# Kernel optimization log

Hardware: AMD Instinct MI355X
Metric: run time of the kernel (lower is better)

Reference implementation:

```python
import jax, jax.numpy as jnp
import numpy as np

# ---- Cl(4,1) Cayley table (signature [1,1,1,1,-1]), basis blades indexed by 5-bit mask ----
_METRIC = np.array([1, 1, 1, 1, -1], dtype=np.float32)

def _build_gp_map():
    T = np.zeros((32, 32, 32), dtype=np.float32)
    for a in range(32):
        for b in range(32):
            # canonical reordering sign (count generator swaps)
            s, aa = 0, a >> 1
            while aa:
                s += bin(aa & b).count('1')
                aa >>= 1
            sign = -1.0 if (s & 1) else 1.0
            # metric contribution of annihilated common generators
            common = a & b
            for i in range(5):
                if (common >> i) & 1:
                    sign *= _METRIC[i]
            T[a, b, a ^ b] = sign  # e_a * e_b = sign * e_{a XOR b}
    return T

GP_MAP = _build_gp_map()  # [32, 32, 32], one signed nonzero per (a,b) pair

IN_FEATURES = 256
OUT_FEATURES = 256
BATCH, SEQ = 4, 512


def setup_inputs() -> dict:
    key = jax.random.key(0)
    kx, kw = jax.random.split(key)
    x = jax.random.normal(kx, (BATCH, SEQ, IN_FEATURES, 32), dtype=jnp.float32)
    # Versor init: std = sqrt(2 / (fan_in * 32))
    std = (2.0 / (IN_FEATURES * 32)) ** 0.5
    weight = jax.random.normal(kw, (OUT_FEATURES, IN_FEATURES, 32), dtype=jnp.float32) * std
    return {"x": x, "weight": weight}


def normalize_cl41(out, eps=1e-6):
    # Normalize each output multivector by its Euclidean norm over the 32 basis coeffs.
    norm = jnp.sqrt(jnp.sum(out * out, axis=-1, keepdims=True) + eps)
    return out / norm


def reference(x, weight):
    gp = jnp.asarray(GP_MAP, dtype=x.dtype)  # [j, l, k]
    # W_op[o,i,l,k] = sum_j weight[o,i,j] * gp[j,l,k]
    W_op = jnp.einsum('oij,jlk->oilk', weight, gp)
    # out[b,s,o,k] = sum_{i,l} x[b,s,i,l] * W_op[o,i,l,k]
    out = jnp.einsum('bsil,oilk->bsok', x, W_op)
    return normalize_cl41(out)
```

## Files before the change

kernel.cpp:

```cpp
#include <hip/hip_runtime.h>
#include <stdint.h>

#define AS1 __attribute__((address_space(1)))
#define AS3 __attribute__((address_space(3)))

typedef __attribute__((ext_vector_type(8))) short bf16x8;
typedef __attribute__((ext_vector_type(4))) float f32x4;


struct Mono { int col[4]; int ph[4]; };

constexpr Mono mono_mul(Mono A, Mono B) {
    Mono R{};
    for (int r = 0; r < 4; ++r) {
        int k = A.col[r];
        R.col[r] = B.col[k];
        R.ph[r] = (A.ph[r] + B.ph[k]) & 3;
    }
    return R;
}

constexpr Mono gen(int g) {
    Mono E{};
    for (int r = 0; r < 4; ++r) {
        int r1 = (r >> 1) & 1, r0 = r & 1;
        if (g == 0)      { E.col[r] = r ^ 2; E.ph[r] = 0; }
        else if (g == 1) { E.col[r] = r ^ 2; E.ph[r] = r1 ? 1 : 3; }
        else if (g == 2) { E.col[r] = r ^ 1; E.ph[r] = r1 ? 2 : 0; }
        else if (g == 3) { E.col[r] = r ^ 1; E.ph[r] = ((r1 ? 2 : 0) + (r0 ? 1 : 3)) & 3; }
        else             { E.col[r] = r;     E.ph[r] = (1 + (r1 ? 2 : 0) + (r0 ? 2 : 0)) & 3; }
    }
    return E;
}

struct Blades { Mono m[32]; };
constexpr Blades make_blades() {
    Blades B{};
    for (int A = 0; A < 32; ++A) {
        Mono M{};
        for (int r = 0; r < 4; ++r) { M.col[r] = r; M.ph[r] = 0; }
        for (int g = 0; g < 5; ++g)
            if ((A >> g) & 1) M = mono_mul(M, gen(g));
        B.m[A] = M;
    }
    return B;
}
constexpr Blades BL = make_blades();

struct FwdTab { int bl[4][4][2][4]; float sg[4][4][2][4]; };
constexpr FwdTab make_fwd() {
    FwdTab T{};
    int cnt[4][4][2] = {};
    for (int A = 0; A < 32; ++A)
        for (int r = 0; r < 4; ++r) {
            int c = BL.m[A].col[r], p = BL.m[A].ph[r];
            int rc = p & 1;
            int& n = cnt[r][c][rc];
            T.bl[r][c][rc][n] = A;
            T.sg[r][c][rc][n] = (p & 2) ? -1.f : 1.f;
            ++n;
        }
    return T;
}
constexpr FwdTab FT = make_fwd();

__device__ inline unsigned short f2bf(float f) {
    uint32_t u = __float_as_uint(f);
    u += 0x7FFFu + ((u >> 16) & 1u);
    return (unsigned short)(u >> 16);
}

__global__ __launch_bounds__(256) void xform_kernel(const float* __restrict__ x,
                                                    const float* __restrict__ w,
                                                    unsigned short* __restrict__ Xb,
                                                    unsigned short* __restrict__ Wr) {
    if (blockIdx.x < 2048) {
        int t = blockIdx.x * 256 + threadIdx.x;
        int i = t & 255, n = t >> 8;
        float v[32];
        const float4* xp = (const float4*)(x + (size_t)t * 32);
#pragma unroll
        for (int q = 0; q < 8; ++q) {
            float4 f = xp[q];
            v[q * 4 + 0] = f.x; v[q * 4 + 1] = f.y; v[q * 4 + 2] = f.z; v[q * 4 + 3] = f.w;
        }
#pragma unroll
        for (int b = 0; b < 4; ++b) {
            union { unsigned short s[8]; uint4 u; } r;
#pragma unroll
            for (int c = 0; c < 4; ++c)
#pragma unroll
                for (int rc = 0; rc < 2; ++rc) {
                    float s = 0.f;
#pragma unroll
                    for (int j = 0; j < 4; ++j)
                        s += FT.sg[c][b][rc][j] * v[FT.bl[c][b][rc][j]];
                    r.s[c * 2 + rc] = f2bf(s);
                }
            *((uint4*)(Xb + (size_t)(n * 4 + b) * 2048 + i * 8)) = r.u;
        }
    } else {
        int t = (blockIdx.x - 2048) * 256 + threadIdx.x;
        int i = t & 255, o = t >> 8;
        float v[32];
        const float4* wp = (const float4*)(w + (size_t)t * 32);
#pragma unroll
        for (int q = 0; q < 8; ++q) {
            float4 f = wp[q];
            v[q * 4 + 0] = f.x; v[q * 4 + 1] = f.y; v[q * 4 + 2] = f.z; v[q * 4 + 3] = f.w;
        }
        float Re[4][4], Im[4][4];
#pragma unroll
        for (int a = 0; a < 4; ++a)
#pragma unroll
            for (int c = 0; c < 4; ++c) {
                float sr = 0.f, si = 0.f;
#pragma unroll
                for (int j = 0; j < 4; ++j) {
                    sr += FT.sg[a][c][0][j] * v[FT.bl[a][c][0][j]];
                    si += FT.sg[a][c][1][j] * v[FT.bl[a][c][1][j]];
                }
                Re[a][c] = sr; Im[a][c] = si;
            }
#pragma unroll
        for (int ra = 0; ra < 2; ++ra)
#pragma unroll
            for (int a = 0; a < 4; ++a) {
                int m = o * 8 + ra * 4 + a;
                union { unsigned short s[8]; uint4 u; } r;
#pragma unroll
                for (int c = 0; c < 4; ++c) {
                    float v0 = ra == 0 ? Re[a][c] : Im[a][c];
                    float v1 = ra == 0 ? -Im[a][c] : Re[a][c];
                    r.s[c * 2 + 0] = f2bf(v0);
                    r.s[c * 2 + 1] = f2bf(v1);
                }
                *((uint4*)(Wr + (size_t)m * 2048 + i * 8)) = r.u;
            }
    }
}

__global__ __launch_bounds__(512, 2) void gemm_kernel(const unsigned short* __restrict__ A,
                                                      const unsigned short* __restrict__ B,
                                                      float* __restrict__ out) {
    const int K = 2048;
    const int NT = 64;
    __shared__ alignas(16) unsigned short SM[4 * 16384];

    const int tid = threadIdx.x;
    const int wid = tid >> 6, lane = tid & 63;
    const int lm = lane & 15, quad = lane >> 4;
    const int wm = wid >> 2, wn = wid & 3;
    const int row0 = blockIdx.y * 256;
    const int col0 = blockIdx.x * 256;

    size_t gA[2], gB[2];
    int ldsA[2], ldsB[2];
#pragma unroll
    for (int p = 0; p < 2; ++p) {
        int g = p * 512 + tid;
        int r = g >> 2, c = g & 3;
        int sc = c ^ ((r >> 1) & 3);
        gA[p] = (size_t)(row0 + r) * K + sc * 8;
        gB[p] = (size_t)(col0 + r) * K + sc * 8;
        ldsA[p] = (p * 512 + wid * 64) * 8;
        ldsB[p] = 8192 + (p * 512 + wid * 64) * 8;
    }

    const int swz = (lm >> 1) & 3;
    const int aoff = (wm * 128 + lm) * 32 + (quad ^ swz) * 8;
    const int boff = 8192 + (wn * 64 + lm) * 32 + (quad ^ swz) * 8;

    f32x4 acc[8][4];
#pragma unroll
    for (int i = 0; i < 8; ++i)
#pragma unroll
        for (int j = 0; j < 4; ++j) acc[i][j] = (f32x4){0.f, 0.f, 0.f, 0.f};

    auto ISSUE = [&](int t) {
        const int bb = (t & 3) * 16384;
        const int k0 = t * 32;
#pragma unroll
        for (int p = 0; p < 2; ++p) {
            __builtin_amdgcn_global_load_lds((const AS1 void*)(A + gA[p] + k0),
                                             (AS3 void*)(&SM[bb + ldsA[p]]), 16, 0, 0);
            __builtin_amdgcn_global_load_lds((const AS1 void*)(B + gB[p] + k0),
                                             (AS3 void*)(&SM[bb + ldsB[p]]), 16, 0, 0);
        }
    };
    auto COMPUTE = [&](int t) {
        const int bb = (t & 3) * 16384;
        bf16x8 av[8], bv[4];
#pragma unroll
        for (int fn = 0; fn < 4; ++fn) bv[fn] = *(const bf16x8*)&SM[bb + boff + fn * 512];
#pragma unroll
        for (int fm = 0; fm < 8; ++fm) av[fm] = *(const bf16x8*)&SM[bb + aoff + fm * 512];
        __builtin_amdgcn_s_setprio(1);
#pragma unroll
        for (int fm = 0; fm < 8; ++fm)
#pragma unroll
            for (int fn = 0; fn < 4; ++fn)
                acc[fm][fn] = __builtin_amdgcn_mfma_f32_16x16x32_bf16(av[fm], bv[fn],
                                                                      acc[fm][fn], 0, 0, 0);
        __builtin_amdgcn_s_setprio(0);
    };

    ISSUE(0); ISSUE(1); ISSUE(2);
    for (int t = 0; t < NT - 3; ++t) {
        asm volatile("s_waitcnt vmcnt(8)" ::: "memory");
        __builtin_amdgcn_s_barrier();
        ISSUE(t + 3);
        COMPUTE(t);
    }
    asm volatile("s_waitcnt vmcnt(8)" ::: "memory");
    __builtin_amdgcn_s_barrier();
    COMPUTE(NT - 3);
    asm volatile("s_waitcnt vmcnt(4)" ::: "memory");
    __builtin_amdgcn_s_barrier();
    COMPUTE(NT - 2);
    asm volatile("s_waitcnt vmcnt(0)" ::: "memory");
    __builtin_amdgcn_s_barrier();
    COMPUTE(NT - 1);
    __syncthreads();

    float* scrw = (float*)SM + wid * 2048;
    const int nl = lane >> 2, ol = lane & 3;
#pragma unroll
    for (int s = 0; s < 4; ++s) {
#pragma unroll
        for (int h = 0; h < 2; ++h)
#pragma unroll
            for (int fn = 0; fn < 4; ++fn)
#pragma unroll
                for (int r = 0; r < 4; ++r) {
                    int rw = h * 16 + quad * 4 + r;
                    int cc = (fn * 16 + lm) ^ (quad << 3);
                    scrw[rw * 64 + cc] = acc[s * 2 + h][fn][r];
                }
        asm volatile("s_waitcnt lgkmcnt(0)" ::: "memory");
        float V[32];
#pragma unroll
        for (int u = 0; u < 8; ++u) {
            int row = ol * 8 + u;
            int cb = (nl * 4) ^ (((row >> 2) & 3) << 3);
            float4 f = *(const float4*)&scrw[row * 64 + cb];
            int vi = (u >> 2) * 16 + (u & 3) * 4;
            V[vi + 0] = f.x; V[vi + 1] = f.y; V[vi + 2] = f.z; V[vi + 3] = f.w;
        }
        float xa[32];
        float ss = 0.f;
#pragma unroll
        for (int Ab = 0; Ab < 32; ++Ab) {
            float sv = 0.f;
#pragma unroll
            for (int a = 0; a < 4; ++a) {
                const int c = BL.m[Ab].col[a];
                const int p = BL.m[Ab].ph[a];
                float vv = V[(p & 1) * 16 + a * 4 + c];
                sv += (p & 2) ? -vv : vv;
            }
            sv *= 0.25f;
            xa[Ab] = sv;
            ss += sv * sv;
        }
        float inv = rsqrtf(ss + 1e-6f);
        int o = (row0 >> 3) + wm * 16 + s * 4 + ol;
        int n = (col0 >> 2) + wn * 16 + nl;
        float4* op = (float4*)(out + ((size_t)n * 256 + o) * 32);
#pragma unroll
        for (int q = 0; q < 8; ++q) {
            float4 f;
            f.x = xa[q * 4 + 0] * inv; f.y = xa[q * 4 + 1] * inv;
            f.z = xa[q * 4 + 2] * inv; f.w = xa[q * 4 + 3] * inv;
            op[q] = f;
        }
        asm volatile("s_waitcnt lgkmcnt(0)" ::: "memory");
    }
}

extern "C" void kernel_launch(void* const* d_in, const int* in_sizes, int n_in,
                              void* d_out, int out_size, void* d_ws, size_t ws_size,
                              hipStream_t stream) {
    const float* x = (const float*)d_in[0];
    const float* w = (const float*)d_in[1];
    float* out = (float*)d_out;

    unsigned short* Wr = (unsigned short*)d_ws;
    unsigned short* Xb = (unsigned short*)((char*)d_ws + 8388608);

    hipLaunchKernelGGL(xform_kernel, dim3(2304),  dim3(256), 0, stream, x, w, Xb, Wr);
    hipLaunchKernelGGL(gemm_kernel,  dim3(32, 8), dim3(512), 0, stream, Wr, Xb, out);
}
```

Before: 194.0 us.

## Restructure GEMM main loop into double-buffered split-slot pipeline; coalesce xform loads via LDS

The GEMM main loop moves from a 4-deep ring of K=32 tiles to two 64-wide K buffers, each split into four slots (A/B halves). Each slot's global-to-LDS load is issued in between half-tile MFMA groups, with extra barriers so loads interleave with compute at a finer grain. The xform kernel now stages x through swizzled shared memory so global reads are fully coalesced instead of per-thread 128-byte strided reads. This adds more barriers per iteration and a shallower prefetch distance in the GEMM, which could expose memory latency.

```diff
diff --git a/kernel.cpp b/kernel.cpp
--- a/kernel.cpp
+++ b/kernel.cpp
@@ -6,7 +6,6 @@
 
 typedef __attribute__((ext_vector_type(8))) short bf16x8;
 typedef __attribute__((ext_vector_type(4))) float f32x4;
-
 
 struct Mono { int col[4]; int ph[4]; };
 
@@ -74,16 +73,29 @@
                                                     const float* __restrict__ w,
                                                     unsigned short* __restrict__ Xb,
                                                     unsigned short* __restrict__ Wr) {
+    __shared__ alignas(16) float XS[8192];
     if (blockIdx.x < 2048) {
-        int t = blockIdx.x * 256 + threadIdx.x;
+        int tid = threadIdx.x;
+        const float4* xp = (const float4*)(x + (size_t)blockIdx.x * 8192);
+        float4 ld[8];
+#pragma unroll
+        for (int r = 0; r < 8; ++r) ld[r] = xp[r * 256 + tid];
+#pragma unroll
+        for (int r = 0; r < 8; ++r) {
+            int U = r * 256 + tid;
+            int L = (U & ~7) | ((U & 7) ^ ((U >> 3) & 7));
+            *(float4*)&XS[L * 4] = ld[r];
+        }
+        __syncthreads();
+        float v[32];
+#pragma unroll
+        for (int q = 0; q < 8; ++q) {
+            int L = tid * 8 + (q ^ (tid & 7));
+            float4 f = *(const float4*)&XS[L * 4];
+            v[q * 4 + 0] = f.x; v[q * 4 + 1] = f.y; v[q * 4 + 2] = f.z; v[q * 4 + 3] = f.w;
+        }
+        int t = blockIdx.x * 256 + tid;
         int i = t & 255, n = t >> 8;
-        float v[32];
-        const float4* xp = (const float4*)(x + (size_t)t * 32);
-#pragma unroll
-        for (int q = 0; q < 8; ++q) {
-            float4 f = xp[q];
-            v[q * 4 + 0] = f.x; v[q * 4 + 1] = f.y; v[q * 4 + 2] = f.z; v[q * 4 + 3] = f.w;
-        }
 #pragma unroll
         for (int b = 0; b < 4; ++b) {
             union { unsigned short s[8]; uint4 u; } r;
@@ -144,8 +156,7 @@
                                                       const unsigned short* __restrict__ B,
                                                       float* __restrict__ out) {
     const int K = 2048;
-    const int NT = 64;
-    __shared__ alignas(16) unsigned short SM[4 * 16384];
+    __shared__ alignas(16) unsigned short SM[65536];
 
     const int tid = threadIdx.x;
     const int wid = tid >> 6, lane = tid & 63;
@@ -155,21 +166,17 @@
     const int col0 = blockIdx.x * 256;
 
     size_t gA[2], gB[2];
-    int ldsA[2], ldsB[2];
 #pragma unroll
     for (int p = 0; p < 2; ++p) {
-        int g = p * 512 + tid;
-        int r = g >> 2, c = g & 3;
-        int sc = c ^ ((r >> 1) & 3);
-        gA[p] = (size_t)(row0 + r) * K + sc * 8;
-        gB[p] = (size_t)(col0 + r) * K + sc * 8;
-        ldsA[p] = (p * 512 + wid * 64) * 8;
-        ldsB[p] = 8192 + (p * 512 + wid * 64) * 8;
+        int u = p * 512 + tid;
+        int r = u >> 2, j = (u & 3) ^ ((r >> 1) & 3);
+        gA[p] = (size_t)(row0 + r) * K + j * 8;
+        gB[p] = (size_t)(col0 + r) * K + j * 8;
     }
 
     const int swz = (lm >> 1) & 3;
     const int aoff = (wm * 128 + lm) * 32 + (quad ^ swz) * 8;
-    const int boff = 8192 + (wn * 64 + lm) * 32 + (quad ^ swz) * 8;
+    const int boff = (wn * 64 + lm) * 32 + (quad ^ swz) * 8;
 
     f32x4 acc[8][4];
 #pragma unroll
@@ -177,50 +184,128 @@
 #pragma unroll
         for (int j = 0; j < 4; ++j) acc[i][j] = (f32x4){0.f, 0.f, 0.f, 0.f};
 
-    auto ISSUE = [&](int t) {
-        const int bb = (t & 3) * 16384;
-        const int k0 = t * 32;
-#pragma unroll
-        for (int p = 0; p < 2; ++p) {
-            __builtin_amdgcn_global_load_lds((const AS1 void*)(A + gA[p] + k0),
-                                             (AS3 void*)(&SM[bb + ldsA[p]]), 16, 0, 0);
-            __builtin_amdgcn_global_load_lds((const AS1 void*)(B + gB[p] + k0),
-                                             (AS3 void*)(&SM[bb + ldsB[p]]), 16, 0, 0);
-        }
+    auto STAGE = [&](int tt, int slot) {
+        const int ks = slot >> 1;
+        const size_t ko = (size_t)tt * 64 + ks * 32;
+        const int dst = (tt & 1) * 32768 + slot * 8192;
+        const unsigned short* base = (slot & 1) ? B : A;
+        const size_t g0 = (slot & 1) ? gB[0] : gA[0];
+        const size_t g1 = (slot & 1) ? gB[1] : gA[1];
+        __builtin_amdgcn_global_load_lds((const AS1 void*)(base + g0 + ko),
+                                         (AS3 void*)&SM[dst + wid * 512], 16, 0, 0);
+        __builtin_amdgcn_global_load_lds((const AS1 void*)(base + g1 + ko),
+                                         (AS3 void*)&SM[dst + 4096 + wid * 512], 16, 0, 0);
     };
-    auto COMPUTE = [&](int t) {
-        const int bb = (t & 3) * 16384;
-        bf16x8 av[8], bv[4];
-#pragma unroll
-        for (int fn = 0; fn < 4; ++fn) bv[fn] = *(const bf16x8*)&SM[bb + boff + fn * 512];
-#pragma unroll
-        for (int fm = 0; fm < 8; ++fm) av[fm] = *(const bf16x8*)&SM[bb + aoff + fm * 512];
-        __builtin_amdgcn_s_setprio(1);
-#pragma unroll
-        for (int fm = 0; fm < 8; ++fm)
-#pragma unroll
-            for (int fn = 0; fn < 4; ++fn)
-                acc[fm][fn] = __builtin_amdgcn_mfma_f32_16x16x32_bf16(av[fm], bv[fn],
-                                                                      acc[fm][fn], 0, 0, 0);
-        __builtin_amdgcn_s_setprio(0);
-    };
-
-    ISSUE(0); ISSUE(1); ISSUE(2);
-    for (int t = 0; t < NT - 3; ++t) {
-        asm volatile("s_waitcnt vmcnt(8)" ::: "memory");
-        __builtin_amdgcn_s_barrier();
-        ISSUE(t + 3);
-        COMPUTE(t);
-    }
-    asm volatile("s_waitcnt vmcnt(8)" ::: "memory");
-    __builtin_amdgcn_s_barrier();
-    COMPUTE(NT - 3);
-    asm volatile("s_waitcnt vmcnt(4)" ::: "memory");
-    __builtin_amdgcn_s_barrier();
-    COMPUTE(NT - 2);
-    asm volatile("s_waitcnt vmcnt(0)" ::: "memory");
-    __builtin_amdgcn_s_barrier();
-    COMPUTE(NT - 1);
+
+    STAGE(0, 0); STAGE(0, 1); STAGE(0, 2); STAGE(0, 3);
+
+    bf16x8 a0[4], a1[4], bv[4];
+    for (int t = 0; t < 31; ++t) {
+        const int bb = (t & 1) * 32768;
+        asm volatile("s_waitcnt vmcnt(4)" ::: "memory");
+        __builtin_amdgcn_s_barrier();
+#pragma unroll
+        for (int f = 0; f < 4; ++f) a0[f] = *(const bf16x8*)&SM[bb + aoff + f * 512];
+#pragma unroll
+        for (int f = 0; f < 4; ++f) bv[f] = *(const bf16x8*)&SM[bb + 8192 + boff + f * 512];
+        STAGE(t + 1, 0);
+        __builtin_amdgcn_s_barrier();
+        __builtin_amdgcn_s_setprio(1);
+#pragma unroll
+        for (int f = 0; f < 4; ++f)
+#pragma unroll
+            for (int n = 0; n < 4; ++n)
+                acc[f][n] = __builtin_amdgcn_mfma_f32_16x16x32_bf16(a0[f], bv[n], acc[f][n], 0, 0, 0);
+        __builtin_amdgcn_s_setprio(0);
+#pragma unroll
+        for (int f = 0; f < 4; ++f) a1[f] = *(const bf16x8*)&SM[bb + aoff + (f + 4) * 512];
+        STAGE(t + 1, 1);
+        __builtin_amdgcn_s_barrier();
+        __builtin_amdgcn_s_setprio(1);
+#pragma unroll
+        for (int f = 0; f < 4; ++f)
+#pragma unroll
+            for (int n = 0; n < 4; ++n)
+                acc[f + 4][n] = __builtin_amdgcn_mfma_f32_16x16x32_bf16(a1[f], bv[n], acc[f + 4][n], 0, 0, 0);
+        __builtin_amdgcn_s_setprio(0);
+        asm volatile("s_waitcnt vmcnt(4)" ::: "memory");
+        __builtin_amdgcn_s_barrier();
+#pragma unroll
+        for (int f = 0; f < 4; ++f) a0[f] = *(const bf16x8*)&SM[bb + 16384 + aoff + f * 512];
+#pragma unroll
+        for (int f = 0; f < 4; ++f) bv[f] = *(const bf16x8*)&SM[bb + 24576 + boff + f * 512];
+        STAGE(t + 1, 2);
+        __builtin_amdgcn_s_barrier();
+        __builtin_amdgcn_s_setprio(1);
+#pragma unroll
+        for (int f = 0; f < 4; ++f)
+#pragma unroll
+            for (int n = 0; n < 4; ++n)
+                acc[f][n] = __builtin_amdgcn_mfma_f32_16x16x32_bf16(a0[f], bv[n], acc[f][n], 0, 0, 0);
+        __builtin_amdgcn_s_setprio(0);
+#pragma unroll
+        for (int f = 0; f < 4; ++f) a1[f] = *(const bf16x8*)&SM[bb + 16384 + aoff + (f + 4) * 512];
+        STAGE(t + 1, 3);
+        __builtin_amdgcn_s_barrier();
+        __builtin_amdgcn_s_setprio(1);
+#pragma unroll
+        for (int f = 0; f < 4; ++f)
+#pragma unroll
+            for (int n = 0; n < 4; ++n)
+                acc[f + 4][n] = __builtin_amdgcn_mfma_f32_16x16x32_bf16(a1[f], bv[n], acc[f + 4][n], 0, 0, 0);
+        __builtin_amdgcn_s_setprio(0);
+    }
+    {
+        const int bb = 32768;
+        asm volatile("s_waitcnt vmcnt(4)" ::: "memory");
+        __builtin_amdgcn_s_barrier();
+#pragma unroll
+        for (int f = 0; f < 4; ++f) a0[f] = *(const bf16x8*)&SM[bb + aoff + f * 512];
+#pragma unroll
+        for (int f = 0; f < 4; ++f) bv[f] = *(const bf16x8*)&SM[bb + 8192 + boff + f * 512];
+        __builtin_amdgcn_s_barrier();
+        __builtin_amdgcn_s_setprio(1);
+#pragma unroll
+        for (int f = 0; f < 4; ++f)
+#pragma unroll
+            for (int n = 0; n < 4; ++n)
+                acc[f][n] = __builtin_amdgcn_mfma_f32_16x16x32_bf16(a0[f], bv[n], acc[f][n], 0, 0, 0);
+        __builtin_amdgcn_s_setprio(0);
+#pragma unroll
+        for (int f = 0; f < 4; ++f) a1[f] = *(const bf16x8*)&SM[bb + aoff + (f + 4) * 512];
+        __builtin_amdgcn_s_barrier();
+        __builtin_amdgcn_s_setprio(1);
+#pragma unroll
+        for (int f = 0; f < 4; ++f)
+#pragma unroll
+            for (int n = 0; n < 4; ++n)
+                acc[f + 4][n] = __builtin_amdgcn_mfma_f32_16x16x32_bf16(a1[f], bv[n], acc[f + 4][n], 0, 0, 0);
+        __builtin_amdgcn_s_setprio(0);
+        asm volatile("s_waitcnt vmcnt(0)" ::: "memory");
+        __builtin_amdgcn_s_barrier();
+#pragma unroll
+        for (int f = 0; f < 4; ++f) a0[f] = *(const bf16x8*)&SM[bb + 16384 + aoff + f * 512];
+#pragma unroll
+        for (int f = 0; f < 4; ++f) bv[f] = *(const bf16x8*)&SM[bb + 24576 + boff + f * 512];
+        __builtin_amdgcn_s_barrier();
+        __builtin_amdgcn_s_setprio(1);
+#pragma unroll
+        for (int f = 0; f < 4; ++f)
+#pragma unroll
+            for (int n = 0; n < 4; ++n)
+                acc[f][n] = __builtin_amdgcn_mfma_f32_16x16x32_bf16(a0[f], bv[n], acc[f][n], 0, 0, 0);
+        __builtin_amdgcn_s_setprio(0);
+#pragma unroll
+        for (int f = 0; f < 4; ++f) a1[f] = *(const bf16x8*)&SM[bb + 16384 + aoff + (f + 4) * 512];
+        __builtin_amdgcn_s_barrier();
+        __builtin_amdgcn_s_setprio(1);
+#pragma unroll
+        for (int f = 0; f < 4; ++f)
+#pragma unroll
+            for (int n = 0; n < 4; ++n)
+                acc[f + 4][n] = __builtin_amdgcn_mfma_f32_16x16x32_bf16(a1[f], bv[n], acc[f + 4][n], 0, 0, 0);
+        __builtin_amdgcn_s_setprio(0);
+    }
     __syncthreads();
 
     float* scrw = (float*)SM + wid * 2048;
```

Measured after the change: 190.7 us. Within noise of the previous version (-1.7%).
